# Optimization experiments

Hardware: AMD Instinct MI355X
Metric: run time of the kernel (lower is better)

## Reference

```python
import jax, jax.numpy as jnp
import numpy as np

SR = 44100
B, T = 4, SR * 3          # batch, samples (duration_secs=3)
NWT, L = 64, 512          # n_wavetables, wavetable_len


def setup_inputs() -> dict:
    key = jax.random.key(0)
    k1, k2, k3, k4, k5 = jax.random.split(key, 5)
    pitch = jax.random.uniform(k1, (B, T, 1), dtype=jnp.float32, minval=50.0, maxval=500.0)
    amplitude = jax.random.uniform(k2, (B, T, 1), dtype=jnp.float32)
    y = jax.random.normal(k3, (B, T), dtype=jnp.float32)
    wavetables = jax.random.normal(k4, (NWT, L), dtype=jnp.float32) * 0.01
    # replicate init: last sample equals first sample of each table
    wavetables = wavetables.at[:, -1].set(wavetables[:, 0])
    conv_w = jax.random.normal(k5, (1, 1, 5), dtype=jnp.float32) * 0.3  # Conv1d(1,1,5)
    conv_b = jnp.zeros((1,), dtype=jnp.float32)
    return {"pitch": pitch, "amplitude": amplitude, "y": y,
            "wavetables": wavetables, "conv_w": conv_w, "conv_b": conv_b,
            "duration_secs": 3}


def reference(pitch, amplitude, y, wavetables, conv_w, conv_b, duration_secs):
    Lwt = wavetables.shape[1]
    freq = pitch.squeeze(-1)                                   # (B, T)
    increment = freq / SR * Lwt                                # (B, T)
    # NOTE: faithful to source: subtract batch-row 0 from every row
    index = jnp.cumsum(increment, axis=1) - increment[0]
    index = index % Lwt
    idx_low = jnp.floor(index)
    idx_high = jnp.ceil(index)
    alpha = index - idx_low                                    # (B, T)
    il = idx_low.astype(jnp.int32)
    ih = idx_high.astype(jnp.int32) % Lwt
    # vectorized over all 64 wavetables at once (source loops in Python)
    low = jnp.take(wavetables, il, axis=1)                     # (N, B, T)
    high = jnp.take(wavetables, ih, axis=1)                    # (N, B, T)
    waveforms = low + alpha * (high - low)                     # (N, B, T)
    # attention: mean over batch of waveform * y
    att = jnp.mean(waveforms * y, axis=1)                      # (N, T)
    att = jax.lax.conv_general_dilated(
        att[:, None, :], conv_w, window_strides=(1,), padding=[(2, 2)],
        dimension_numbers=("NCH", "OIH", "NCH"))[:, 0, :] + conv_b[0]
    att = jax.nn.softmax(att, axis=0)                          # softmax over wavetables
    out = jnp.einsum("nbt,nt->bt", waveforms, att)             # (B, T)
    out = out[..., None] * amplitude                           # (B, T, 1)
    return out
```

## Files before the change

kernel.cpp:

```cpp
#include <hip/hip_runtime.h>
#include <math.h>

#define LWT 512
#define NWT 64
#define BB 4
#define SBASE 16
#define WAVES 9
#define THREADS (WAVES * 64)
#define PSTRIDE 18


#define INC_C ((float)(512.0 / 44100.0))

__device__ __forceinline__ float inc_mul(float p) {
  float v = p * INC_C;
  asm volatile("" : "+v"(v));
  return v;
}
__device__ __forceinline__ float inc_of(const float* p, int t) { return inc_mul(p[t]); }

__global__ void __launch_bounds__(256) scan_level0(const float* __restrict__ pitch,
                                                   float* __restrict__ sarr,
                                                   float* __restrict__ s1g,
                                                   int T, int NB1) {
  int k = blockIdx.x * blockDim.x + threadIdx.x;
  int b = blockIdx.y;
  if (k >= NB1) return;
  const float* prow = pitch + (size_t)b * T;
  float* srow = sarr + (size_t)b * T;
  int t0 = k * SBASE;
  float run = 0.0f;
  if (t0 + SBASE <= T) {
    const float4* p4 = reinterpret_cast<const float4*>(prow + t0);
    float4* s4o = reinterpret_cast<float4*>(srow + t0);
#pragma unroll
    for (int i = 0; i < 4; ++i) {
      float4 v = p4[i];
      float4 o;
      run += inc_mul(v.x); o.x = run;
      run += inc_mul(v.y); o.y = run;
      run += inc_mul(v.z); o.z = run;
      run += inc_mul(v.w); o.w = run;
      s4o[i] = o;
    }
  } else {
    for (int t = t0; t < T; ++t) { run += inc_of(prow, t); srow[t] = run; }
  }
  s1g[(size_t)b * NB1 + k] = run;
}

__global__ void __launch_bounds__(1024) scan_mid(float* __restrict__ s1g,
                                                 float* __restrict__ s2g,
                                                 int NB1, int NB2) {
  int b = blockIdx.x, tid = threadIdx.x;
  float* s1r = s1g + (size_t)b * NB1;
  __shared__ float s2[544];
  __shared__ float s3[48];
  __shared__ float s4[16];
  const int NB3 = (NB2 + SBASE - 1) / SBASE;
  const int NB4 = (NB3 + SBASE - 1) / SBASE;
  if (tid < NB2) {
    int a0 = tid * SBASE, a1 = a0 + SBASE < NB1 ? a0 + SBASE : NB1;
    float run = 0.0f;
    for (int a = a0; a < a1; ++a) { run += s1r[a]; s1r[a] = run; }
    s2[tid] = run;
  }
  __syncthreads();
  if (tid < NB3) {
    int a0 = tid * SBASE, a1 = a0 + SBASE < NB2 ? a0 + SBASE : NB2;
    float run = 0.0f;
    for (int a = a0; a < a1; ++a) { run += s2[a]; s2[a] = run; }
    s3[tid] = run;
  }
  __syncthreads();
  if (tid < NB4) {
    int a0 = tid * SBASE, a1 = a0 + SBASE < NB3 ? a0 + SBASE : NB3;
    float run = 0.0f;
    for (int a = a0; a < a1; ++a) { run += s3[a]; s3[a] = run; }
    s4[tid] = run;
  }
  __syncthreads();
  if (tid == 0) { float r = 0.0f; for (int a = 0; a < NB4; ++a) { r += s4[a]; s4[a] = r; } }
  __syncthreads();
  if (tid < NB3 && tid >= SBASE) s3[tid] = s3[tid] + s4[tid / SBASE - 1];
  __syncthreads();
  if (tid < NB2) {
    float v = s2[tid];
    if (tid >= SBASE) v = v + s3[tid / SBASE - 1];
    s2g[(size_t)b * NB2 + tid] = v;
  }
}

__device__ __forceinline__ float shdn1(float x, bool edge) {
  int xi = __float_as_int(x);
  int a = __builtin_amdgcn_update_dpp(0, xi, 0x111, 0xf, 0xf, true);
  int b = __builtin_amdgcn_update_dpp(0, xi, 0x142, 0xf, 0xf, true);
  return __int_as_float(edge ? b : a);
}

__global__ void __launch_bounds__(THREADS) fused_out(
    const float* __restrict__ pitch, const float* __restrict__ sarr,
    const float* __restrict__ s1g, const float* __restrict__ s2g,
    const float* __restrict__ y, const float* __restrict__ amp,
    const float* __restrict__ wt, const float* __restrict__ cw,
    const float* __restrict__ cb, float* __restrict__ out,
    int T, int NB1, int NB2) {
  __shared__ float lds_pairs[512 * PSTRIDE];
  int wid = threadIdx.x >> 6, lane = threadIdx.x & 63;
  const bool edge = (lane & 15) == 0;
  int seg = wid * 256 + blockIdx.x;
  const int NSEG = (T + 59) / 60;
  bool segv = seg < NSEG;
  int ta = seg * 60 - 2 + lane;

  int loi0 = 0, loi1 = 0, loi2 = 0, loi3 = 0;
  float alf[BB] = {0.f, 0.f, 0.f, 0.f};
  float yv[BB] = {0.f, 0.f, 0.f, 0.f};
  if (segv && ta >= 0 && ta < T) {
#pragma unroll
    for (int b = 0; b < BB; ++b) {
      float S = sarr[(size_t)b * T + ta];
      if (ta >= SBASE) {
        int k1 = (ta >> 4) - 1;
        float s1v = s1g[b * NB1 + k1];
        if (k1 >= SBASE) s1v = s1v + s2g[b * NB2 + (k1 >> 4) - 1];
        S = S + s1v;
      }
      float iv = S - inc_of(pitch, ta);
      float q = iv * (1.0f / 512.0f);
      float k = floorf(q);
      iv = fmaf(-k, 512.0f, iv);
      float fl = floorf(iv);
      float alpha = iv - fl;
      int ili = (int)fl; if (ili > 511) ili = 511;
      int lo = ili * PSTRIDE;
      if (b == 0) loi0 = lo;
      else if (b == 1) loi1 = lo;
      else if (b == 2) loi2 = lo;
      else loi3 = lo;
      alf[b] = alpha;
      yv[b] = y[(size_t)b * T + ta];
    }
  }

  float w0 = cw[0], w1 = cw[1], w2 = cw[2], w3 = cw[3], w4 = cw[4];
  float bias = cb[0];
  float r0 = 0.f, r1 = 0.f, r2 = 0.f, r3 = 0.f, ssum = 0.f;

  for (int h = 0; h < 8; ++h) {
    __syncthreads();
    for (int idx = threadIdx.x; idx < 512 * 8; idx += THREADS) {
      int nl = idx >> 9;
      int c = idx & 511;
      int ng = h * 8 + nl;
      float lo = wt[ng * 512 + c];
      float hi = wt[ng * 512 + ((c + 1) & 511)];
      *reinterpret_cast<float2*>(&lds_pairs[c * PSTRIDE + 2 * nl]) =
          make_float2(lo, hi - lo);
    }
    __syncthreads();
    if (segv) {
#pragma unroll
      for (int nl = 0; nl < 8; ++nl) {
        float2 p0 = *reinterpret_cast<const float2*>(&lds_pairs[loi0 + 2 * nl]);
        float2 p1 = *reinterpret_cast<const float2*>(&lds_pairs[loi1 + 2 * nl]);
        float2 p2 = *reinterpret_cast<const float2*>(&lds_pairs[loi2 + 2 * nl]);
        float2 p3 = *reinterpret_cast<const float2*>(&lds_pairs[loi3 + 2 * nl]);
        float wv0 = fmaf(alf[0], p0.y, p0.x);
        float wv1 = fmaf(alf[1], p1.y, p1.x);
        float wv2 = fmaf(alf[2], p2.y, p2.x);
        float wv3 = fmaf(alf[3], p3.y, p3.x);
        float acc = wv0 * yv[0];
        acc += wv1 * yv[1];
        acc += wv2 * yv[2];
        acc += wv3 * yv[3];
        acc *= 0.25f;
        float d1 = shdn1(acc, edge);
        float d2 = shdn1(d1, edge);
        float d3 = shdn1(d2, edge);
        float d4 = shdn1(d3, edge);
        float c0 = bias + d4 * w0 + d3 * w1 + d2 * w2 + d1 * w3 + acc * w4;
        float e = __expf(c0);
        float s0 = shdn1(shdn1(wv0, edge), edge);
        float s1 = shdn1(shdn1(wv1, edge), edge);
        float s2 = shdn1(shdn1(wv2, edge), edge);
        float s3 = shdn1(shdn1(wv3, edge), edge);
        r0 += e * s0;
        r1 += e * s1;
        r2 += e * s2;
        r3 += e * s3;
        ssum += e;
      }
    }
  }

  if (segv && lane >= 4) {
    int tout = ta - 2;
    if (tout < T) {
#if __has_builtin(__builtin_amdgcn_rcpf)
      float rc = __builtin_amdgcn_rcpf(ssum);
#else
      float rc = 1.0f / ssum;
#endif
      out[(size_t)0 * T + tout] = r0 * rc * amp[(size_t)0 * T + tout];
      out[(size_t)1 * T + tout] = r1 * rc * amp[(size_t)1 * T + tout];
      out[(size_t)2 * T + tout] = r2 * rc * amp[(size_t)2 * T + tout];
      out[(size_t)3 * T + tout] = r3 * rc * amp[(size_t)3 * T + tout];
    }
  }
}

extern "C" void kernel_launch(void* const* d_in, const int* in_sizes, int n_in,
                              void* d_out, int out_size, void* d_ws, size_t ws_size,
                              hipStream_t stream) {
  const float* pitch = (const float*)d_in[0];
  const float* amp   = (const float*)d_in[1];
  const float* y     = (const float*)d_in[2];
  const float* wt    = (const float*)d_in[3];
  const float* cw    = (const float*)d_in[4];
  const float* cb    = (const float*)d_in[5];
  float* out = (float*)d_out;

  int BT = in_sizes[2];
  int T = BT / BB;
  int NB1 = (T + SBASE - 1) / SBASE;
  int NB2 = (NB1 + SBASE - 1) / SBASE;

  float* ws   = (float*)d_ws;
  float* sarr = ws;
  float* s1g  = ws + (size_t)BT;
  float* s2g  = s1g + (size_t)BB * NB1;

  hipLaunchKernelGGL(scan_level0, dim3((NB1 + 255) / 256, BB), dim3(256), 0, stream,
                     pitch, sarr, s1g, T, NB1);
  hipLaunchKernelGGL(scan_mid, dim3(BB), dim3(1024), 0, stream, s1g, s2g, NB1, NB2);
  hipLaunchKernelGGL(fused_out, dim3(256), dim3(THREADS), 0, stream,
                     pitch, sarr, s1g, s2g, y, amp, wt, cw, cb, out, T, NB1, NB2);
}
```

Measured before the change: 57.80 us.

## Remap fused kernel to 4-wave blocks and shuffle exp weights instead of waveforms

The fused kernel now launches many small 4-wave blocks, each covering contiguous 60-sample segments, instead of 256 blocks of 9 waves with strided segment assignment. The softmax weight is moved to the output lane with one lane shuffle, replacing eight DPP shifts of the four waveform values. The wavetable LDS stride changes to an odd 17 with scalar loads to cut bank conflicts, and the 0.25 mean factor is folded into y. The trade-off is more blocks that each re-stage the full wavetable into LDS, which adds L2 traffic and staging iterations per block.

New measurement: 58.34 us. Within noise of the previous version (+0.9%).

```diff
diff --git a/kernel.cpp b/kernel.cpp
--- a/kernel.cpp
+++ b/kernel.cpp
@@ -5,9 +5,10 @@
 #define NWT 64
 #define BB 4
 #define SBASE 16
-#define WAVES 9
-#define THREADS (WAVES * 64)
-#define PSTRIDE 18
+#define TPW 60
+#define WPB 4
+#define TPB (TPW * WPB)
+#define PSTR 17
 
 
 #define INC_C ((float)(512.0 / 44100.0))
@@ -98,20 +99,20 @@
   return __int_as_float(edge ? b : a);
 }
 
-__global__ void __launch_bounds__(THREADS) fused_out(
+__global__ void __launch_bounds__(WPB * 64) fused_out(
     const float* __restrict__ pitch, const float* __restrict__ sarr,
     const float* __restrict__ s1g, const float* __restrict__ s2g,
     const float* __restrict__ y, const float* __restrict__ amp,
     const float* __restrict__ wt, const float* __restrict__ cw,
     const float* __restrict__ cb, float* __restrict__ out,
     int T, int NB1, int NB2) {
-  __shared__ float lds_pairs[512 * PSTRIDE];
+  __shared__ float lds_wt[512 * PSTR];
   int wid = threadIdx.x >> 6, lane = threadIdx.x & 63;
   const bool edge = (lane & 15) == 0;
-  int seg = wid * 256 + blockIdx.x;
-  const int NSEG = (T + 59) / 60;
-  bool segv = seg < NSEG;
-  int ta = seg * 60 - 2 + lane;
+  int seg = blockIdx.x * WPB + wid;
+  bool segv = (size_t)seg * TPW < (size_t)T;
+  int tw = seg * TPW;
+  int ta = tw - 2 + lane;
 
   int loi0 = 0, loi1 = 0, loi2 = 0, loi3 = 0;
   float alf[BB] = {0.f, 0.f, 0.f, 0.f};
@@ -133,13 +134,13 @@
       float fl = floorf(iv);
       float alpha = iv - fl;
       int ili = (int)fl; if (ili > 511) ili = 511;
-      int lo = ili * PSTRIDE;
+      int lo = ili * PSTR;
       if (b == 0) loi0 = lo;
       else if (b == 1) loi1 = lo;
       else if (b == 2) loi2 = lo;
       else loi3 = lo;
       alf[b] = alpha;
-      yv[b] = y[(size_t)b * T + ta];
+      yv[b] = y[(size_t)b * T + ta] * 0.25f;
     }
   }
 
@@ -149,64 +150,58 @@
 
   for (int h = 0; h < 8; ++h) {
     __syncthreads();
-    for (int idx = threadIdx.x; idx < 512 * 8; idx += THREADS) {
+    for (int idx = threadIdx.x; idx < 512 * 8; idx += WPB * 64) {
       int nl = idx >> 9;
       int c = idx & 511;
       int ng = h * 8 + nl;
       float lo = wt[ng * 512 + c];
       float hi = wt[ng * 512 + ((c + 1) & 511)];
-      *reinterpret_cast<float2*>(&lds_pairs[c * PSTRIDE + 2 * nl]) =
-          make_float2(lo, hi - lo);
+      lds_wt[c * PSTR + 2 * nl] = lo;
+      lds_wt[c * PSTR + 2 * nl + 1] = hi - lo;
     }
     __syncthreads();
     if (segv) {
 #pragma unroll
       for (int nl = 0; nl < 8; ++nl) {
-        float2 p0 = *reinterpret_cast<const float2*>(&lds_pairs[loi0 + 2 * nl]);
-        float2 p1 = *reinterpret_cast<const float2*>(&lds_pairs[loi1 + 2 * nl]);
-        float2 p2 = *reinterpret_cast<const float2*>(&lds_pairs[loi2 + 2 * nl]);
-        float2 p3 = *reinterpret_cast<const float2*>(&lds_pairs[loi3 + 2 * nl]);
-        float wv0 = fmaf(alf[0], p0.y, p0.x);
-        float wv1 = fmaf(alf[1], p1.y, p1.x);
-        float wv2 = fmaf(alf[2], p2.y, p2.x);
-        float wv3 = fmaf(alf[3], p3.y, p3.x);
+        float lo0 = lds_wt[loi0 + 2 * nl], sl0 = lds_wt[loi0 + 2 * nl + 1];
+        float lo1 = lds_wt[loi1 + 2 * nl], sl1 = lds_wt[loi1 + 2 * nl + 1];
+        float lo2 = lds_wt[loi2 + 2 * nl], sl2 = lds_wt[loi2 + 2 * nl + 1];
+        float lo3 = lds_wt[loi3 + 2 * nl], sl3 = lds_wt[loi3 + 2 * nl + 1];
+        float wv0 = fmaf(alf[0], sl0, lo0);
+        float wv1 = fmaf(alf[1], sl1, lo1);
+        float wv2 = fmaf(alf[2], sl2, lo2);
+        float wv3 = fmaf(alf[3], sl3, lo3);
         float acc = wv0 * yv[0];
         acc += wv1 * yv[1];
         acc += wv2 * yv[2];
         acc += wv3 * yv[3];
-        acc *= 0.25f;
         float d1 = shdn1(acc, edge);
         float d2 = shdn1(d1, edge);
         float d3 = shdn1(d2, edge);
         float d4 = shdn1(d3, edge);
         float c0 = bias + d4 * w0 + d3 * w1 + d2 * w2 + d1 * w3 + acc * w4;
         float e = __expf(c0);
-        float s0 = shdn1(shdn1(wv0, edge), edge);
-        float s1 = shdn1(shdn1(wv1, edge), edge);
-        float s2 = shdn1(shdn1(wv2, edge), edge);
-        float s3 = shdn1(shdn1(wv3, edge), edge);
-        r0 += e * s0;
-        r1 += e * s1;
-        r2 += e * s2;
-        r3 += e * s3;
+        float esh = __shfl(e, lane + 2);
+        r0 = fmaf(esh, wv0, r0);
+        r1 = fmaf(esh, wv1, r1);
+        r2 = fmaf(esh, wv2, r2);
+        r3 = fmaf(esh, wv3, r3);
         ssum += e;
       }
     }
   }
 
-  if (segv && lane >= 4) {
-    int tout = ta - 2;
-    if (tout < T) {
+  float ssum_sh = __shfl(ssum, lane + 2);
+  if (segv && lane >= 2 && lane < 62 && ta < T) {
 #if __has_builtin(__builtin_amdgcn_rcpf)
-      float rc = __builtin_amdgcn_rcpf(ssum);
+    float rc = __builtin_amdgcn_rcpf(ssum_sh);
 #else
-      float rc = 1.0f / ssum;
+    float rc = 1.0f / ssum_sh;
 #endif
-      out[(size_t)0 * T + tout] = r0 * rc * amp[(size_t)0 * T + tout];
-      out[(size_t)1 * T + tout] = r1 * rc * amp[(size_t)1 * T + tout];
-      out[(size_t)2 * T + tout] = r2 * rc * amp[(size_t)2 * T + tout];
-      out[(size_t)3 * T + tout] = r3 * rc * amp[(size_t)3 * T + tout];
-    }
+    out[(size_t)0 * T + ta] = r0 * rc * amp[(size_t)0 * T + ta];
+    out[(size_t)1 * T + ta] = r1 * rc * amp[(size_t)1 * T + ta];
+    out[(size_t)2 * T + ta] = r2 * rc * amp[(size_t)2 * T + ta];
+    out[(size_t)3 * T + ta] = r3 * rc * amp[(size_t)3 * T + ta];
   }
 }
 
@@ -234,6 +229,6 @@
   hipLaunchKernelGGL(scan_level0, dim3((NB1 + 255) / 256, BB), dim3(256), 0, stream,
                      pitch, sarr, s1g, T, NB1);
   hipLaunchKernelGGL(scan_mid, dim3(BB), dim3(1024), 0, stream, s1g, s2g, NB1, NB2);
-  hipLaunchKernelGGL(fused_out, dim3(256), dim3(THREADS), 0, stream,
+  hipLaunchKernelGGL(fused_out, dim3((T + TPB - 1) / TPB), dim3(WPB * 64), 0, stream,
                      pitch, sarr, s1g, s2g, y, amp, wt, cw, cb, out, T, NB1, NB2);
 }
```
